# Kernel optimization log

Measured on AMD Instinct MI355X. Metric: run time of the kernel, lower is better.

The kernel has to match this reference:

```python
import jax, jax.numpy as jnp
import numpy as np

B, N, E, F, C = 4, 10000, 160000, 128, 128
NUM_ITERATIONS = 3  # num_iterations init arg


def setup_inputs() -> dict:
    key = jax.random.key(0)
    ks = jax.random.split(key, 8)
    objects = jax.random.normal(ks[0], (B, N, F), dtype=jnp.float32)
    connections = jax.random.randint(ks[1], (B, E, 2), 0, N, dtype=jnp.int32)
    # small init scales keep exp() in the attention numerically tame (mirrors
    # glorot/orthogonal-scale weights at init)
    object_state_W = jax.random.normal(ks[2], (F, C), dtype=jnp.float32) * (1.0 / np.sqrt(F))
    state_attention_W = jax.random.normal(ks[3], (C, C), dtype=jnp.float32) * 0.05
    linked_state_attention_W = jax.random.normal(ks[4], (C, C), dtype=jnp.float32) * 0.05
    linked_state_W = jax.random.normal(ks[5], (C, C), dtype=jnp.float32) * (1.0 / np.sqrt(C))
    attention_b = jnp.zeros((C,), dtype=jnp.float32)
    state_b = jnp.zeros((C,), dtype=jnp.float32)
    return {
        "objects": objects,
        "object_state_W": object_state_W,
        "state_attention_W": state_attention_W,
        "linked_state_attention_W": linked_state_attention_W,
        "attention_b": attention_b,
        "linked_state_W": linked_state_W,
        "state_b": state_b,
        "connections": connections,
    }


def reference(objects, object_state_W, state_attention_W, linked_state_attention_W,
              attention_b, linked_state_W, state_b, connections):
    # bidirectional: double edges with both orientations  [B, 2E]
    src = jnp.concatenate([connections[:, :, 0], connections[:, :, 1]], axis=1)
    dst = jnp.concatenate([connections[:, :, 1], connections[:, :, 0]], axis=1)

    # initial states: [B, N, C]
    states = jnp.tanh(jnp.einsum('bnf,fc->bnc', objects, object_state_W) + state_b)

    def step_one(states_b, src_b, dst_b):
        # states_b: [N, C]; src_b/dst_b: [2E]
        states_aW = states_b @ state_attention_W          # [N, C]
        linked_aW = states_b @ linked_state_attention_W   # [N, C]
        # per-edge unnormalized attention  [2E, C]
        attention = jnp.exp(states_aW[src_b] + linked_aW[dst_b] + attention_b)
        # scatter-add normalization; self edge contributes 1 (exp(0))
        attention_norm = jnp.ones_like(states_b).at[src_b].add(attention)  # [N, C]
        self_attention = 1.0 / attention_norm
        attention = attention / attention_norm[src_b]
        # weighted neighbor aggregation
        attented = attention * states_b[dst_b]                              # [2E, C]
        linked_gated = jnp.zeros_like(states_b).at[src_b].add(attented)     # [N, C]
        return jnp.tanh(states_b * self_attention + linked_gated @ linked_state_W + state_b)

    step = jax.vmap(step_one)
    for _ in range(NUM_ITERATIONS):
        states = step(states, src, dst)
    return states
```

## Files before the change

kernel.cpp:

```cpp
#include <hip/hip_runtime.h>
#include <hip/hip_bf16.h>


#define BATCH 4
#define NNODE 10000
#define NEDGE 160000
#define TWOE  (2*NEDGE)
#define MROWS (BATCH*NNODE)
#define NCHUNK 64
#define CHUNKE (NEDGE/NCHUNK)
#define PADN  10240

typedef unsigned short u16;
typedef unsigned int   u32;
typedef __attribute__((ext_vector_type(8))) short bf16x8_t;
typedef __attribute__((ext_vector_type(4))) float f32x4_t;

__device__ __forceinline__ float b2f(u16 h){ return __uint_as_float(((u32)h) << 16); }
__device__ __forceinline__ u16 f2bf(float f){
  u32 u = __float_as_uint(f);
  return (u16)((u + 0x7fffu + ((u >> 16) & 1u)) >> 16);
}
__device__ __forceinline__ float fast_tanh(float x){
  float e = __expf(2.0f * x);
  return fmaf(-2.0f, __builtin_amdgcn_rcpf(e + 1.0f), 1.0f);
}

__global__ void detect_dtype(const u32* __restrict__ objw, int* __restrict__ flag){
  __shared__ int zc, hc;
  if (threadIdx.x == 0){ zc = 0; hc = 0; }
  __syncthreads();
  int z = 0, h = 0;
  for (int i = threadIdx.x; i < 1024; i += 256){
    u32 lo = objw[i] & 0xffffu;
    if (lo == 0) z++;
    if (((lo >> 7) & 0xffu) >= 160u) h++;
  }
  atomicAdd(&zc, z); atomicAdd(&hc, h);
  __syncthreads();
  if (threadIdx.x == 0) *flag = (hc > 0 || zc > 512) ? 1 : 0;
}

__global__ void prep_weights(const void* __restrict__ Wo, const void* __restrict__ Wa,
                             const void* __restrict__ Wla, const void* __restrict__ Wl,
                             const void* __restrict__ ab, const void* __restrict__ sb,
                             const int* __restrict__ flag, u16* __restrict__ Wt,
                             float* __restrict__ biasf){
  int idx = blockIdx.x * 256 + threadIdx.x;
  bool f = (*flag != 0);
  if (idx < 65536){
    int m = idx >> 14, k = (idx >> 7) & 127, c = idx & 127;
    const void* src = (m == 0) ? Wo : (m == 1) ? Wa : (m == 2) ? Wla : Wl;
    u16 h = f ? f2bf(((const float*)src)[k * 128 + c]) : ((const u16*)src)[k * 128 + c];
    Wt[m * 16384 + c * 128 + k] = h;
  } else {
    int t = idx - 65536;
    const void* src = (t < 128) ? sb : ab;
    int i = t & 127;
    biasf[t] = f ? ((const float*)src)[i] : b2f(((const u16*)src)[i]);
  }
}

__device__ __forceinline__ void chunk_of(int blk, int& b, int& c){
  int xcd = blk & 7;
  b = xcd >> 1;
  c = ((blk >> 3) << 1) | (xcd & 1);
}

__global__ void __launch_bounds__(256) csr_hist(const int* __restrict__ conn,
                                                u16* __restrict__ partial){
  int b, c; chunk_of(blockIdx.x, b, c);
  __shared__ u32 hist[NNODE];
  for (int n = threadIdx.x; n < NNODE; n += 256) hist[n] = 0;
  __syncthreads();
  const int2* cp = (const int2*)conn + (size_t)b * NEDGE + c * CHUNKE;
  for (int i = threadIdx.x; i < CHUNKE; i += 256){
    int2 e = cp[i];
    atomicAdd(&hist[e.x], 1);
    atomicAdd(&hist[e.y], 1);
  }
  __syncthreads();
  u16* prow = partial + (size_t)(b * NCHUNK + c) * PADN;
  for (int n = threadIdx.x; n < NNODE; n += 256) prow[n] = (u16)hist[n];
}

__global__ void __launch_bounds__(256) csr_colscan(u16* __restrict__ partial,
    int* __restrict__ row_start, int* __restrict__ bsum){
  int b = blockIdx.x / 40, w = blockIdx.x % 40;
  int n = w * 256 + threadIdx.x;
  u32 run = 0;
  if (n < NNODE){
    #pragma unroll 8
    for (int c = 0; c < NCHUNK; c++){
      size_t idx = (size_t)(b * NCHUNK + c) * PADN + n;
      u32 v = partial[idx];
      partial[idx] = (u16)run;
      run += v;
    }
  }
  __shared__ u32 buf[256];
  buf[threadIdx.x] = run;
  __syncthreads();
  for (int off = 1; off < 256; off <<= 1){
    u32 x = (threadIdx.x >= (unsigned)off) ? buf[threadIdx.x - off] : 0;
    __syncthreads();
    buf[threadIdx.x] += x;
    __syncthreads();
  }
  u32 incl = buf[threadIdx.x];
  if (n < NNODE) row_start[b * (NNODE + 1) + n] = (int)(incl - run);
  if (threadIdx.x == 255) bsum[blockIdx.x] = (int)incl;
}

__global__ void scanB(const int* __restrict__ bsum, int* __restrict__ boff,
                      int* __restrict__ row_start){
  __shared__ int s[160];
  if (threadIdx.x < 160) s[threadIdx.x] = bsum[threadIdx.x];
  __syncthreads();
  if (threadIdx.x < 160){
    int b = threadIdx.x / 40, j = threadIdx.x % 40;
    int off = 0;
    for (int q = b * 40; q < b * 40 + j; q++) off += s[q];
    boff[threadIdx.x] = off;
  }
  if (threadIdx.x < BATCH) row_start[threadIdx.x * (NNODE + 1) + NNODE] = TWOE;
}

__global__ void scanC(int* __restrict__ row_start, const int* __restrict__ boff){
  int b = blockIdx.x / 40, j = blockIdx.x % 40;
  int n = j * 256 + threadIdx.x;
  if (n < NNODE) row_start[b * (NNODE + 1) + n] += boff[blockIdx.x];
}

__global__ void __launch_bounds__(256) csr_fill(const int* __restrict__ conn,
    const u16* __restrict__ partial, const int* __restrict__ row_start,
    int* __restrict__ edge_dst){
  int b, c; chunk_of(blockIdx.x, b, c);
  __shared__ u32 cur[NNODE];
  const u16* prow = partial + (size_t)(b * NCHUNK + c) * PADN;
  const int* rs = row_start + b * (NNODE + 1);
  for (int n = threadIdx.x; n < NNODE; n += 256) cur[n] = (u32)rs[n] + prow[n];
  __syncthreads();
  const int2* cp = (const int2*)conn + (size_t)b * NEDGE + c * CHUNKE;
  int* edb = edge_dst + (size_t)b * TWOE;
  for (int i = threadIdx.x; i < CHUNKE; i += 256){
    int2 e = cp[i];
    u32 p1 = atomicAdd(&cur[e.x], 1); edb[p1] = e.y;
    u32 p2 = atomicAdd(&cur[e.y], 1); edb[p2] = e.x;
  }
}

__device__ __forceinline__ void gemm_tile(const u16* __restrict__ arow,
    const u16* __restrict__ wt, int lm, int lq, f32x4_t acc[8]){
  #pragma unroll
  for (int ks = 0; ks < 4; ks++){
    bf16x8_t a = *(const bf16x8_t*)(arow + ks * 32);
    #pragma unroll
    for (int nb = 0; nb < 8; nb++){
      bf16x8_t bfr = *(const bf16x8_t*)(wt + (nb * 16 + lm) * 128 + ks * 32 + lq * 8);
      acc[nb] = __builtin_amdgcn_mfma_f32_16x16x32_bf16(a, bfr, acc[nb], 0, 0, 0);
    }
  }
}

__device__ __forceinline__ void gemm_tile_packed(const u32* __restrict__ Lrow,
    const u16* __restrict__ wt, int lm, int lq, f32x4_t acc[8]){
  #pragma unroll
  for (int ks = 0; ks < 4; ks++){
    uint4 wa = *(const uint4*)(Lrow + ks * 32 + lq * 8);
    uint4 wb = *(const uint4*)(Lrow + ks * 32 + lq * 8 + 4);
    bf16x8_t a;
    a[0] = (short)wa.x; a[1] = (short)wa.y; a[2] = (short)wa.z; a[3] = (short)wa.w;
    a[4] = (short)wb.x; a[5] = (short)wb.y; a[6] = (short)wb.z; a[7] = (short)wb.w;
    #pragma unroll
    for (int nb = 0; nb < 8; nb++){
      bf16x8_t bfr = *(const bf16x8_t*)(wt + (nb * 16 + lm) * 128 + ks * 32 + lq * 8);
      acc[nb] = __builtin_amdgcn_mfma_f32_16x16x32_bf16(a, bfr, acc[nb], 0, 0, 0);
    }
  }
}

__device__ __forceinline__ void phase2_awlaw(const u16* __restrict__ ldsrow,
    const u16* __restrict__ Wt, const float* __restrict__ biasf,
    int lm, int lq, int r0, float* __restrict__ awsa,
    u32* __restrict__ gat0, u32* __restrict__ gat1){
  const u16* Wta  = Wt + 16384;
  const u16* Wtla = Wt + 32768;
  f32x4_t accA[8], accL[8];
  #pragma unroll
  for (int i = 0; i < 8; i++){ accA[i] = (f32x4_t){0.f,0.f,0.f,0.f}; accL[i] = (f32x4_t){0.f,0.f,0.f,0.f}; }
  #pragma unroll
  for (int ks = 0; ks < 4; ks++){
    bf16x8_t a = *(const bf16x8_t*)(ldsrow + ks * 32);
    #pragma unroll
    for (int nb = 0; nb < 8; nb++){
      bf16x8_t ba = *(const bf16x8_t*)(Wta  + (nb * 16 + lm) * 128 + ks * 32 + lq * 8);
      bf16x8_t bl = *(const bf16x8_t*)(Wtla + (nb * 16 + lm) * 128 + ks * 32 + lq * 8);
      accA[nb] = __builtin_amdgcn_mfma_f32_16x16x32_bf16(a, ba, accA[nb], 0, 0, 0);
      accL[nb] = __builtin_amdgcn_mfma_f32_16x16x32_bf16(a, bl, accL[nb], 0, 0, 0);
    }
  }
  #pragma unroll
  for (int nb = 0; nb < 8; nb++){
    int col = nb * 16 + lm;
    u16* gh = (u16*)((nb < 4) ? gat0 : gat1);
    float bb = biasf[128 + col];
    #pragma unroll
    for (int i = 0; i < 4; i++){
      int row = r0 + lq * 4 + i;
      awsa[(size_t)row * 128 + col] = accA[nb][i];
      gh[((size_t)row * 64 + (col & 63)) * 2] = f2bf(__expf(accL[nb][i] + bb));
    }
  }
}

__global__ void __launch_bounds__(256) fused_init(const void* __restrict__ obj_raw,
    const int* __restrict__ flag, const u16* __restrict__ Wt,
    const float* __restrict__ biasf, float* __restrict__ awsa,
    u32* __restrict__ gat0, u32* __restrict__ gat1){
  __shared__ u16 lds[4][16][136];
  const int lane = threadIdx.x & 63, wave = threadIdx.x >> 6;
  const int r0 = blockIdx.x * 64 + wave * 16;
  const int lm = lane & 15, lq = lane >> 4;
  f32x4_t acc[8];
  #pragma unroll
  for (int i = 0; i < 8; i++) acc[i] = (f32x4_t){0.f, 0.f, 0.f, 0.f};
  if (*flag){
    const float* arow = (const float*)obj_raw + (size_t)(r0 + lm) * 128 + lq * 8;
    #pragma unroll
    for (int ks = 0; ks < 4; ks++){
      float4 fa = *(const float4*)(arow + ks * 32);
      float4 fb = *(const float4*)(arow + ks * 32 + 4);
      bf16x8_t a;
      a[0] = (short)f2bf(fa.x); a[1] = (short)f2bf(fa.y);
      a[2] = (short)f2bf(fa.z); a[3] = (short)f2bf(fa.w);
      a[4] = (short)f2bf(fb.x); a[5] = (short)f2bf(fb.y);
      a[6] = (short)f2bf(fb.z); a[7] = (short)f2bf(fb.w);
      #pragma unroll
      for (int nb = 0; nb < 8; nb++){
        bf16x8_t bfr = *(const bf16x8_t*)(Wt + (nb * 16 + lm) * 128 + ks * 32 + lq * 8);
        acc[nb] = __builtin_amdgcn_mfma_f32_16x16x32_bf16(a, bfr, acc[nb], 0, 0, 0);
      }
    }
  } else {
    gemm_tile((const u16*)obj_raw + (size_t)(r0 + lm) * 128 + lq * 8, Wt, lm, lq, acc);
  }
  #pragma unroll
  for (int nb = 0; nb < 8; nb++){
    int col = nb * 16 + lm;
    u16* gh = (u16*)((nb < 4) ? gat0 : gat1);
    float bb = biasf[col];
    #pragma unroll
    for (int i = 0; i < 4; i++){
      int row = r0 + lq * 4 + i;
      u16 h = f2bf(fast_tanh(acc[nb][i] + bb));
      gh[((size_t)row * 64 + (col & 63)) * 2 + 1] = h;
      lds[wave][lq * 4 + i][col] = h;
    }
  }
  __syncthreads();
  phase2_awlaw(&lds[wave][lm][lq * 8], Wt, biasf, lm, lq, r0, awsa, gat0, gat1);
}

__global__ void __launch_bounds__(256) fused_mid(const u32* __restrict__ lgsa,
    const u16* __restrict__ Wt, const float* __restrict__ biasf,
    float* __restrict__ awsa, u32* __restrict__ gat0, u32* __restrict__ gat1){
  __shared__ u16 lds[4][16][136];
  const int lane = threadIdx.x & 63, wave = threadIdx.x >> 6;
  const int r0 = blockIdx.x * 64 + wave * 16;
  const int lm = lane & 15, lq = lane >> 4;
  f32x4_t acc[8];
  #pragma unroll
  for (int i = 0; i < 8; i++) acc[i] = (f32x4_t){0.f, 0.f, 0.f, 0.f};
  gemm_tile_packed(lgsa + (size_t)(r0 + lm) * 128, Wt + 49152, lm, lq, acc);
  #pragma unroll
  for (int nb = 0; nb < 8; nb++){
    int col = nb * 16 + lm;
    u16* gh = (u16*)((nb < 4) ? gat0 : gat1);
    float bb = biasf[col];
    #pragma unroll
    for (int i = 0; i < 4; i++){
      int row = r0 + lq * 4 + i;
      u32 v = lgsa[(size_t)row * 128 + col];
      u16 hb = (u16)(v >> 16);
      float sa = (float)(*(const _Float16*)&hb);
      u16 h = f2bf(fast_tanh(sa + acc[nb][i] + bb));
      gh[((size_t)row * 64 + (col & 63)) * 2 + 1] = h;
      lds[wave][lq * 4 + i][col] = h;
    }
  }
  __syncthreads();
  phase2_awlaw(&lds[wave][lm][lq * 8], Wt, biasf, lm, lq, r0, awsa, gat0, gat1);
}

__global__ void __launch_bounds__(256) final_out(const u32* __restrict__ lgsa,
    const u16* __restrict__ Wt, const float* __restrict__ biasf,
    const int* __restrict__ flag, void* __restrict__ outp){
  const int lane = threadIdx.x & 63, wave = threadIdx.x >> 6;
  const int r0 = blockIdx.x * 64 + wave * 16;
  const int lm = lane & 15, lq = lane >> 4;
  bool f32out = (*flag != 0);
  f32x4_t acc[8];
  #pragma unroll
  for (int i = 0; i < 8; i++) acc[i] = (f32x4_t){0.f, 0.f, 0.f, 0.f};
  gemm_tile_packed(lgsa + (size_t)(r0 + lm) * 128, Wt + 49152, lm, lq, acc);
  #pragma unroll
  for (int nb = 0; nb < 8; nb++){
    int col = nb * 16 + lm;
    float bb = biasf[col];
    #pragma unroll
    for (int i = 0; i < 4; i++){
      int row = r0 + lq * 4 + i;
      u32 vv = lgsa[(size_t)row * 128 + col];
      u16 hb = (u16)(vv >> 16);
      float sa = (float)(*(const _Float16*)&hb);
      float v = fast_tanh(sa + acc[nb][i] + bb);
      if (f32out) ((float*)outp)[(size_t)row * 128 + col] = v;
      else        ((u16*)  outp)[(size_t)row * 128 + col] = f2bf(v);
    }
  }
}

__device__ __forceinline__ void acc_e(u32 g, float& s1, float& s2){
  float el = __uint_as_float(g << 16);
  float sv = __uint_as_float(g & 0xffff0000u);
  s1 += el;
  s2 = fmaf(el, sv, s2);
}

__global__ void __launch_bounds__(256) edge_kernel(const float* __restrict__ awsa,
    const u32* __restrict__ gat0, const u32* __restrict__ gat1,
    const int* __restrict__ row_start, const int* __restrict__ edge_dst,
    u32* __restrict__ lgsa){
  int blk = blockIdx.x;
  int xcd = blk & 7;
  int b = xcd >> 1, h = xcd & 1;
  int i = blk >> 3;
  int n = i * 4 + (int)(threadIdx.x >> 6);
  int node = b * NNODE + n;
  int c = threadIdx.x & 63;
  const u32* gh = (h ? gat1 : gat0) + (size_t)b * NNODE * 64;
  int e0 = __builtin_amdgcn_readfirstlane(row_start[b * (NNODE + 1) + n]);
  int e1 = __builtin_amdgcn_readfirstlane(row_start[b * (NNODE + 1) + n + 1]);
  const int* ed = edge_dst + (size_t)b * TWOE;

  float aw = awsa[(size_t)node * 128 + h * 64 + c];
  float ea = __expf(aw);
  float s1 = 0.f, s2 = 0.f, t1 = 0.f, t2 = 0.f;
  int e = e0;
  for (; e + 8 <= e1; e += 8){
    int d0 = ed[e+0], d1 = ed[e+1], d2 = ed[e+2], d3 = ed[e+3];
    int d4 = ed[e+4], d5 = ed[e+5], d6 = ed[e+6], d7 = ed[e+7];
    u32 g0 = gh[(size_t)d0 * 64 + c];
    u32 g1 = gh[(size_t)d1 * 64 + c];
    u32 g2 = gh[(size_t)d2 * 64 + c];
    u32 g3 = gh[(size_t)d3 * 64 + c];
    u32 g4 = gh[(size_t)d4 * 64 + c];
    u32 g5 = gh[(size_t)d5 * 64 + c];
    u32 g6 = gh[(size_t)d6 * 64 + c];
    u32 g7 = gh[(size_t)d7 * 64 + c];
    acc_e(g0, s1, s2); acc_e(g1, t1, t2);
    acc_e(g2, s1, s2); acc_e(g3, t1, t2);
    acc_e(g4, s1, s2); acc_e(g5, t1, t2);
    acc_e(g6, s1, s2); acc_e(g7, t1, t2);
  }
  for (; e < e1; e++){
    u32 gg = gh[(size_t)ed[e] * 64 + c];
    acc_e(gg, s1, s2);
  }
  s1 += t1; s2 += t2;
  float inv = __builtin_amdgcn_rcpf(fmaf(ea, s1, 1.0f));
  float lg = ea * s2 * inv;
  u32 self = gh[(size_t)n * 64 + c];
  float s_self = __uint_as_float(self & 0xffff0000u);
  _Float16 hs = (_Float16)(s_self * inv);
  u32 pk = (u32)f2bf(lg) | ((u32)(*(const u16*)&hs) << 16);
  lgsa[(size_t)node * 128 + h * 64 + c] = pk;
}

extern "C" void kernel_launch(void* const* d_in, const int* in_sizes, int n_in,
                              void* d_out, int out_size, void* d_ws, size_t ws_size,
                              hipStream_t stream){
  (void)in_sizes; (void)n_in; (void)ws_size; (void)out_size;
  const void* objects = d_in[0];
  const void* Wo      = d_in[1];
  const void* Wa      = d_in[2];
  const void* Wla     = d_in[3];
  const void* attn_b  = d_in[4];
  const void* Wl      = d_in[5];
  const void* state_b = d_in[6];
  const int*  conn    = (const int*)d_in[7];

  char* base = (char*)d_ws;
  size_t off = 0;
  auto alloc = [&](size_t bytes) -> char* {
    char* p = base + off;
    off = (off + bytes + 255) & ~(size_t)255;
    return p;
  };
  int*   flag      = (int*)  alloc(256);
  u16*   Wt        = (u16*)  alloc((size_t)4 * 16384 * 2);
  float* biasf     = (float*)alloc(256 * 4);
  float* awsa      = (float*)alloc((size_t)MROWS * 128 * 4);
  u32*   gat0      = (u32*)  alloc((size_t)MROWS * 64 * 4);
  u32*   gat1      = (u32*)  alloc((size_t)MROWS * 64 * 4);
  u32*   lgsa      = (u32*)  alloc((size_t)MROWS * 128 * 4);
  u16*   partial   = (u16*)  alloc((size_t)BATCH * NCHUNK * PADN * 2);
  int*   row_start = (int*)  alloc((size_t)BATCH * (NNODE + 1) * 4);
  int*   edge_dst  = (int*)  alloc((size_t)BATCH * TWOE * 4);
  int*   bsum      = (int*)  alloc(160 * 4);
  int*   boff      = (int*)  alloc(160 * 4);

  detect_dtype<<<1, 256, 0, stream>>>((const u32*)objects, flag);
  prep_weights<<<257, 256, 0, stream>>>(Wo, Wa, Wla, Wl, attn_b, state_b, flag, Wt, biasf);

  csr_hist<<<256, 256, 0, stream>>>(conn, partial);
  csr_colscan<<<160, 256, 0, stream>>>(partial, row_start, bsum);
  scanB<<<1, 256, 0, stream>>>(bsum, boff, row_start);
  scanC<<<160, 256, 0, stream>>>(row_start, boff);
  csr_fill<<<256, 256, 0, stream>>>(conn, partial, row_start, edge_dst);

  fused_init<<<MROWS / 64, 256, 0, stream>>>(objects, flag, Wt, biasf, awsa, gat0, gat1);
  edge_kernel<<<MROWS / 2, 256, 0, stream>>>(awsa, gat0, gat1, row_start, edge_dst, lgsa);
  fused_mid<<<MROWS / 64, 256, 0, stream>>>(lgsa, Wt, biasf, awsa, gat0, gat1);
  edge_kernel<<<MROWS / 2, 256, 0, stream>>>(awsa, gat0, gat1, row_start, edge_dst, lgsa);
  fused_mid<<<MROWS / 64, 256, 0, stream>>>(lgsa, Wt, biasf, awsa, gat0, gat1);
  edge_kernel<<<MROWS / 2, 256, 0, stream>>>(awsa, gat0, gat1, row_start, edge_dst, lgsa);
  final_out<<<MROWS / 64, 256, 0, stream>>>(lgsa, Wt, biasf, flag, d_out);
}
```

Before: 417.0 us.

## Split node GEMM tiles across column halves and pack gather writes

Each 16-row tile is now shared by two waves, each computing 64 of the 128 output columns, so a block covers 32 rows and the grid doubles in size. The two waves exchange the new state through shared memory before the attention GEMMs. The exp(linked) and state halves are now written as one packed 32-bit word instead of two separate 16-bit stores. The aim is more waves in flight and fewer accumulator registers per wave for the small per-node GEMMs, at the cost of the A-operand row being loaded twice per tile.

```diff
diff --git a/kernel.cpp b/kernel.cpp
--- a/kernel.cpp
+++ b/kernel.cpp
@@ -150,21 +150,21 @@
   }
 }
 
-__device__ __forceinline__ void gemm_tile(const u16* __restrict__ arow,
-    const u16* __restrict__ wt, int lm, int lq, f32x4_t acc[8]){
+__device__ __forceinline__ void gemm_tile4(const u16* __restrict__ arow,
+    const u16* __restrict__ wt, int lm, int lq, int cofs, f32x4_t acc[4]){
   #pragma unroll
   for (int ks = 0; ks < 4; ks++){
     bf16x8_t a = *(const bf16x8_t*)(arow + ks * 32);
     #pragma unroll
-    for (int nb = 0; nb < 8; nb++){
-      bf16x8_t bfr = *(const bf16x8_t*)(wt + (nb * 16 + lm) * 128 + ks * 32 + lq * 8);
+    for (int nb = 0; nb < 4; nb++){
+      bf16x8_t bfr = *(const bf16x8_t*)(wt + (cofs + nb * 16 + lm) * 128 + ks * 32 + lq * 8);
       acc[nb] = __builtin_amdgcn_mfma_f32_16x16x32_bf16(a, bfr, acc[nb], 0, 0, 0);
     }
   }
 }
 
-__device__ __forceinline__ void gemm_tile_packed(const u32* __restrict__ Lrow,
-    const u16* __restrict__ wt, int lm, int lq, f32x4_t acc[8]){
+__device__ __forceinline__ void gemm_tile4_packed(const u32* __restrict__ Lrow,
+    const u16* __restrict__ wt, int lm, int lq, int cofs, f32x4_t acc[4]){
   #pragma unroll
   for (int ks = 0; ks < 4; ks++){
     uint4 wa = *(const uint4*)(Lrow + ks * 32 + lq * 8);
@@ -173,43 +173,45 @@
     a[0] = (short)wa.x; a[1] = (short)wa.y; a[2] = (short)wa.z; a[3] = (short)wa.w;
     a[4] = (short)wb.x; a[5] = (short)wb.y; a[6] = (short)wb.z; a[7] = (short)wb.w;
     #pragma unroll
-    for (int nb = 0; nb < 8; nb++){
-      bf16x8_t bfr = *(const bf16x8_t*)(wt + (nb * 16 + lm) * 128 + ks * 32 + lq * 8);
+    for (int nb = 0; nb < 4; nb++){
+      bf16x8_t bfr = *(const bf16x8_t*)(wt + (cofs + nb * 16 + lm) * 128 + ks * 32 + lq * 8);
       acc[nb] = __builtin_amdgcn_mfma_f32_16x16x32_bf16(a, bfr, acc[nb], 0, 0, 0);
     }
   }
 }
 
-__device__ __forceinline__ void phase2_awlaw(const u16* __restrict__ ldsrow,
+__device__ __forceinline__ void phase2_awlaw4(const u16* __restrict__ ldstile,
     const u16* __restrict__ Wt, const float* __restrict__ biasf,
-    int lm, int lq, int r0, float* __restrict__ awsa,
-    u32* __restrict__ gat0, u32* __restrict__ gat1){
+    int lm, int lq, int cofs, int r0, float* __restrict__ awsa,
+    u32* __restrict__ ghw){
   const u16* Wta  = Wt + 16384;
   const u16* Wtla = Wt + 32768;
-  f32x4_t accA[8], accL[8];
-  #pragma unroll
-  for (int i = 0; i < 8; i++){ accA[i] = (f32x4_t){0.f,0.f,0.f,0.f}; accL[i] = (f32x4_t){0.f,0.f,0.f,0.f}; }
+  const u16* ldsrow = ldstile + lm * 136 + lq * 8;
+  f32x4_t accA[4], accL[4];
+  #pragma unroll
+  for (int i = 0; i < 4; i++){ accA[i] = (f32x4_t){0.f,0.f,0.f,0.f}; accL[i] = (f32x4_t){0.f,0.f,0.f,0.f}; }
   #pragma unroll
   for (int ks = 0; ks < 4; ks++){
     bf16x8_t a = *(const bf16x8_t*)(ldsrow + ks * 32);
     #pragma unroll
-    for (int nb = 0; nb < 8; nb++){
-      bf16x8_t ba = *(const bf16x8_t*)(Wta  + (nb * 16 + lm) * 128 + ks * 32 + lq * 8);
-      bf16x8_t bl = *(const bf16x8_t*)(Wtla + (nb * 16 + lm) * 128 + ks * 32 + lq * 8);
+    for (int nb = 0; nb < 4; nb++){
+      bf16x8_t ba = *(const bf16x8_t*)(Wta  + (cofs + nb * 16 + lm) * 128 + ks * 32 + lq * 8);
+      bf16x8_t bl = *(const bf16x8_t*)(Wtla + (cofs + nb * 16 + lm) * 128 + ks * 32 + lq * 8);
       accA[nb] = __builtin_amdgcn_mfma_f32_16x16x32_bf16(a, ba, accA[nb], 0, 0, 0);
       accL[nb] = __builtin_amdgcn_mfma_f32_16x16x32_bf16(a, bl, accL[nb], 0, 0, 0);
     }
   }
   #pragma unroll
-  for (int nb = 0; nb < 8; nb++){
-    int col = nb * 16 + lm;
-    u16* gh = (u16*)((nb < 4) ? gat0 : gat1);
+  for (int nb = 0; nb < 4; nb++){
+    int col = cofs + nb * 16 + lm;
     float bb = biasf[128 + col];
     #pragma unroll
     for (int i = 0; i < 4; i++){
       int row = r0 + lq * 4 + i;
       awsa[(size_t)row * 128 + col] = accA[nb][i];
-      gh[((size_t)row * 64 + (col & 63)) * 2] = f2bf(__expf(accL[nb][i] + bb));
+      u16 el = f2bf(__expf(accL[nb][i] + bb));
+      u16 s  = ldstile[(lq * 4 + i) * 136 + col];
+      ghw[(size_t)row * 64 + (col & 63)] = (u32)el | ((u32)s << 16);
     }
   }
 }
@@ -218,13 +220,14 @@
     const int* __restrict__ flag, const u16* __restrict__ Wt,
     const float* __restrict__ biasf, float* __restrict__ awsa,
     u32* __restrict__ gat0, u32* __restrict__ gat1){
-  __shared__ u16 lds[4][16][136];
+  __shared__ u16 lds[2][16 * 136];
   const int lane = threadIdx.x & 63, wave = threadIdx.x >> 6;
-  const int r0 = blockIdx.x * 64 + wave * 16;
+  const int t = wave >> 1, ch = wave & 1, cofs = ch * 64;
+  const int r0 = blockIdx.x * 32 + t * 16;
   const int lm = lane & 15, lq = lane >> 4;
-  f32x4_t acc[8];
-  #pragma unroll
-  for (int i = 0; i < 8; i++) acc[i] = (f32x4_t){0.f, 0.f, 0.f, 0.f};
+  f32x4_t acc[4];
+  #pragma unroll
+  for (int i = 0; i < 4; i++) acc[i] = (f32x4_t){0.f, 0.f, 0.f, 0.f};
   if (*flag){
     const float* arow = (const float*)obj_raw + (size_t)(r0 + lm) * 128 + lq * 8;
     #pragma unroll
@@ -237,46 +240,41 @@
       a[4] = (short)f2bf(fb.x); a[5] = (short)f2bf(fb.y);
       a[6] = (short)f2bf(fb.z); a[7] = (short)f2bf(fb.w);
       #pragma unroll
-      for (int nb = 0; nb < 8; nb++){
-        bf16x8_t bfr = *(const bf16x8_t*)(Wt + (nb * 16 + lm) * 128 + ks * 32 + lq * 8);
+      for (int nb = 0; nb < 4; nb++){
+        bf16x8_t bfr = *(const bf16x8_t*)(Wt + (cofs + nb * 16 + lm) * 128 + ks * 32 + lq * 8);
         acc[nb] = __builtin_amdgcn_mfma_f32_16x16x32_bf16(a, bfr, acc[nb], 0, 0, 0);
       }
     }
   } else {
-    gemm_tile((const u16*)obj_raw + (size_t)(r0 + lm) * 128 + lq * 8, Wt, lm, lq, acc);
-  }
-  #pragma unroll
-  for (int nb = 0; nb < 8; nb++){
-    int col = nb * 16 + lm;
-    u16* gh = (u16*)((nb < 4) ? gat0 : gat1);
+    gemm_tile4((const u16*)obj_raw + (size_t)(r0 + lm) * 128 + lq * 8, Wt, lm, lq, cofs, acc);
+  }
+  #pragma unroll
+  for (int nb = 0; nb < 4; nb++){
+    int col = cofs + nb * 16 + lm;
     float bb = biasf[col];
     #pragma unroll
-    for (int i = 0; i < 4; i++){
-      int row = r0 + lq * 4 + i;
-      u16 h = f2bf(fast_tanh(acc[nb][i] + bb));
-      gh[((size_t)row * 64 + (col & 63)) * 2 + 1] = h;
-      lds[wave][lq * 4 + i][col] = h;
-    }
-  }
-  __syncthreads();
-  phase2_awlaw(&lds[wave][lm][lq * 8], Wt, biasf, lm, lq, r0, awsa, gat0, gat1);
+    for (int i = 0; i < 4; i++)
+      lds[t][(lq * 4 + i) * 136 + col] = f2bf(fast_tanh(acc[nb][i] + bb));
+  }
+  __syncthreads();
+  phase2_awlaw4(&lds[t][0], Wt, biasf, lm, lq, cofs, r0, awsa, ch ? gat1 : gat0);
 }
 
 __global__ void __launch_bounds__(256) fused_mid(const u32* __restrict__ lgsa,
     const u16* __restrict__ Wt, const float* __restrict__ biasf,
     float* __restrict__ awsa, u32* __restrict__ gat0, u32* __restrict__ gat1){
-  __shared__ u16 lds[4][16][136];
+  __shared__ u16 lds[2][16 * 136];
   const int lane = threadIdx.x & 63, wave = threadIdx.x >> 6;
-  const int r0 = blockIdx.x * 64 + wave * 16;
+  const int t = wave >> 1, ch = wave & 1, cofs = ch * 64;
+  const int r0 = blockIdx.x * 32 + t * 16;
   const int lm = lane & 15, lq = lane >> 4;
-  f32x4_t acc[8];
-  #pragma unroll
-  for (int i = 0; i < 8; i++) acc[i] = (f32x4_t){0.f, 0.f, 0.f, 0.f};
-  gemm_tile_packed(lgsa + (size_t)(r0 + lm) * 128, Wt + 49152, lm, lq, acc);
-  #pragma unroll
-  for (int nb = 0; nb < 8; nb++){
-    int col = nb * 16 + lm;
-    u16* gh = (u16*)((nb < 4) ? gat0 : gat1);
+  f32x4_t acc[4];
+  #pragma unroll
+  for (int i = 0; i < 4; i++) acc[i] = (f32x4_t){0.f, 0.f, 0.f, 0.f};
+  gemm_tile4_packed(lgsa + (size_t)(r0 + lm) * 128, Wt + 49152, lm, lq, cofs, acc);
+  #pragma unroll
+  for (int nb = 0; nb < 4; nb++){
+    int col = cofs + nb * 16 + lm;
     float bb = biasf[col];
     #pragma unroll
     for (int i = 0; i < 4; i++){
@@ -284,29 +282,28 @@
       u32 v = lgsa[(size_t)row * 128 + col];
       u16 hb = (u16)(v >> 16);
       float sa = (float)(*(const _Float16*)&hb);
-      u16 h = f2bf(fast_tanh(sa + acc[nb][i] + bb));
-      gh[((size_t)row * 64 + (col & 63)) * 2 + 1] = h;
-      lds[wave][lq * 4 + i][col] = h;
-    }
-  }
-  __syncthreads();
-  phase2_awlaw(&lds[wave][lm][lq * 8], Wt, biasf, lm, lq, r0, awsa, gat0, gat1);
+      lds[t][(lq * 4 + i) * 136 + col] = f2bf(fast_tanh(sa + acc[nb][i] + bb));
+    }
+  }
+  __syncthreads();
+  phase2_awlaw4(&lds[t][0], Wt, biasf, lm, lq, cofs, r0, awsa, ch ? gat1 : gat0);
 }
 
 __global__ void __launch_bounds__(256) final_out(const u32* __restrict__ lgsa,
     const u16* __restrict__ Wt, const float* __restrict__ biasf,
     const int* __restrict__ flag, void* __restrict__ outp){
   const int lane = threadIdx.x & 63, wave = threadIdx.x >> 6;
-  const int r0 = blockIdx.x * 64 + wave * 16;
+  const int t = wave >> 1, ch = wave & 1, cofs = ch * 64;
+  const int r0 = blockIdx.x * 32 + t * 16;
   const int lm = lane & 15, lq = lane >> 4;
   bool f32out = (*flag != 0);
-  f32x4_t acc[8];
-  #pragma unroll
-  for (int i = 0; i < 8; i++) acc[i] = (f32x4_t){0.f, 0.f, 0.f, 0.f};
-  gemm_tile_packed(lgsa + (size_t)(r0 + lm) * 128, Wt + 49152, lm, lq, acc);
-  #pragma unroll
-  for (int nb = 0; nb < 8; nb++){
-    int col = nb * 16 + lm;
+  f32x4_t acc[4];
+  #pragma unroll
+  for (int i = 0; i < 4; i++) acc[i] = (f32x4_t){0.f, 0.f, 0.f, 0.f};
+  gemm_tile4_packed(lgsa + (size_t)(r0 + lm) * 128, Wt + 49152, lm, lq, cofs, acc);
+  #pragma unroll
+  for (int nb = 0; nb < 4; nb++){
+    int col = cofs + nb * 16 + lm;
     float bb = biasf[col];
     #pragma unroll
     for (int i = 0; i < 4; i++){
@@ -420,11 +417,11 @@
   scanC<<<160, 256, 0, stream>>>(row_start, boff);
   csr_fill<<<256, 256, 0, stream>>>(conn, partial, row_start, edge_dst);
 
-  fused_init<<<MROWS / 64, 256, 0, stream>>>(objects, flag, Wt, biasf, awsa, gat0, gat1);
+  fused_init<<<MROWS / 32, 256, 0, stream>>>(objects, flag, Wt, biasf, awsa, gat0, gat1);
   edge_kernel<<<MROWS / 2, 256, 0, stream>>>(awsa, gat0, gat1, row_start, edge_dst, lgsa);
-  fused_mid<<<MROWS / 64, 256, 0, stream>>>(lgsa, Wt, biasf, awsa, gat0, gat1);
+  fused_mid<<<MROWS / 32, 256, 0, stream>>>(lgsa, Wt, biasf, awsa, gat0, gat1);
   edge_kernel<<<MROWS / 2, 256, 0, stream>>>(awsa, gat0, gat1, row_start, edge_dst, lgsa);
-  fused_mid<<<MROWS / 64, 256, 0, stream>>>(lgsa, Wt, biasf, awsa, gat0, gat1);
+  fused_mid<<<MROWS / 32, 256, 0, stream>>>(lgsa, Wt, biasf, awsa, gat0, gat1);
   edge_kernel<<<MROWS / 2, 256, 0, stream>>>(awsa, gat0, gat1, row_start, edge_dst, lgsa);
-  final_out<<<MROWS / 64, 256, 0, stream>>>(lgsa, Wt, biasf, flag, d_out);
-}
+  final_out<<<MROWS / 32, 256, 0, stream>>>(lgsa, Wt, biasf, flag, d_out);
+}
```

After: 411.5 us. No clear change (-1.3%).
